# Optimization experiments

Hardware: AMD Instinct MI355X
Metric: run time of the kernel (lower is better)

The kernel has to match this reference:

```python
import jax, jax.numpy as jnp
import numpy as np

B, N, C = 8, 4096, 512
H, DK, DV = 8, 64, 64


def _xnorm(x, gamma):
    # L2 norm over last dim, keepdim; scale by per-head gamma
    nrm = jnp.sqrt(jnp.sum(x * x, axis=-1, keepdims=True))
    return x * gamma / nrm


def setup_inputs() -> dict:
    key = jax.random.key(0)
    ks = jax.random.split(key, 9)
    inp = {
        "queries": jax.random.normal(ks[0], (B, N, C), dtype=jnp.float32),
        "keys": jax.random.normal(ks[1], (B, N, C), dtype=jnp.float32),
        "values": jax.random.normal(ks[2], (B, N, C), dtype=jnp.float32),
        # Linear weights stored torch-style [out, in]; init.normal_(std=0.001), bias=0
        "Wq": jax.random.normal(ks[3], (H * DK, C), dtype=jnp.float32) * 0.001,
        "bq": jnp.zeros((H * DK,), dtype=jnp.float32),
        "Wk": jax.random.normal(ks[4], (H * DK, C), dtype=jnp.float32) * 0.001,
        "bk": jnp.zeros((H * DK,), dtype=jnp.float32),
        "Wv": jax.random.normal(ks[5], (H * DV, C), dtype=jnp.float32) * 0.001,
        "bv": jnp.zeros((H * DV,), dtype=jnp.float32),
        "Wo": jax.random.normal(ks[6], (C, H * DV), dtype=jnp.float32) * 0.001,
        "bo": jnp.zeros((C,), dtype=jnp.float32),
        "gamma": jax.random.normal(ks[7], (1, H, 1, 1), dtype=jnp.float32),
    }
    return inp


def reference(queries, keys, values, Wq, bq, Wk, bk, Wv, bv, Wo, bo, gamma):
    bs, nq, _ = queries.shape
    nk = keys.shape[1]
    # projections -> [b, h, n, d]
    q = (queries @ Wq.T + bq).reshape(bs, nq, H, DK).transpose(0, 2, 1, 3)
    k = (keys @ Wk.T + bk).reshape(bs, nk, H, DK).transpose(0, 2, 1, 3)
    v = (values @ Wv.T + bv).reshape(bs, nk, H, DV).transpose(0, 2, 1, 3)
    # kv: [b, h, dk, dv]  (small intermediate)
    kv = jnp.einsum('bhnk,bhnv->bhkv', k, v)
    kv_n = _xnorm(kv, gamma)     # norm over dv
    q_n = _xnorm(q, gamma)       # norm over dk
    out = jnp.einsum('bhnk,bhkv->bhnv', q_n, kv_n)  # [b,h,nq,dv]
    out = out.transpose(0, 2, 1, 3).reshape(bs, nq, H * DV)
    return out @ Wo.T + bo
```

## Files before the change

### kernel.cpp

```cpp
#include <hip/hip_runtime.h>


typedef __attribute__((ext_vector_type(4))) float f32x4;
typedef __attribute__((ext_vector_type(8))) short s16x8;
typedef __attribute__((ext_vector_type(4))) unsigned short u16x4;
typedef __attribute__((ext_vector_type(2))) unsigned u32x2;

#define DEVFN __device__ __forceinline__

DEVFN unsigned short f2b(float f) {
  union { float f; unsigned u; } un; un.f = f;
  unsigned r = un.u + 0x7fffu + ((un.u >> 16) & 1u);
  return (unsigned short)(r >> 16);
}
DEVFN float b2f(unsigned short us) {
  union { unsigned u; float f; } un; un.u = ((unsigned)us) << 16;
  return un.f;
}
DEVFN unsigned pk2(float x0, float x1) {
  union { float f; unsigned u; } a, b;
  a.f = x0; b.f = x1;
  return __builtin_amdgcn_perm(b.u + 0x8000u, a.u + 0x8000u, 0x07060302u);
}

DEVFN void gl_lds16(const void* g, void* l) {
  __builtin_amdgcn_global_load_lds(
      (const __attribute__((address_space(1))) unsigned*)g,
      (__attribute__((address_space(3))) unsigned*)l, 16, 0, 0);
}

template <bool AF32, typename CT>
DEVFN void gemm_core(const void* Ain, const unsigned short* Bt,
                     const float* bias, CT* C, bool qnorm, const float* gamma,
                     int bx, int by) {
  constexpr int NN = 512;
  __shared__ __align__(16) char AsL[2][8192];
  __shared__ __align__(16) char BsL[2][8192];
  const int tid = threadIdx.x, lane = tid & 63, wid = tid >> 6;
  const int wm = (wid >> 1) * 64, wn = (wid & 1) * 64;
  const int r = lane & 15, g = lane >> 4;

  const char* Bsrc = (const char*)Bt +
      (long)(by * 128 + wid * 32 + (lane >> 2)) * 1024 +
      (((lane & 3) ^ ((lane >> 3) & 3)) * 16);

  const char* AsrcR = nullptr;
  const char* AsrcG = nullptr;
  int awr[4];
  if constexpr (AF32) {
    AsrcR = (const char*)Ain + (long)(bx * 128 + (tid >> 1)) * 2048 +
            (tid & 1) * 64;
    const int row = tid >> 1, rs = (row >> 1) & 3;
#pragma unroll
    for (int j = 0; j < 4; ++j) {
      int p = (tid & 1) * 4 + j;
      awr[j] = row * 64 + ((((p >> 1) ^ rs) << 4) | ((p & 1) * 8));
    }
  } else {
    AsrcG = (const char*)Ain +
        (long)(bx * 128 + wid * 32 + (lane >> 2)) * 1024 +
        (((lane & 3) ^ ((lane >> 3) & 3)) * 16);
  }

  f32x4 PA[4];
  f32x4 acc[4][4] = {};

#define ISSUE_A(KT)                                                            \
  {                                                                            \
    _Pragma("unroll") for (int j = 0; j < 4; ++j)                              \
        PA[j] = *reinterpret_cast<const f32x4*>(AsrcR + (KT)*128 + j * 16);    \
  }

#define PACK_WRITE_A(BUF)                                                      \
  {                                                                            \
    _Pragma("unroll") for (int j = 0; j < 4; ++j) {                            \
      u32x2 w;                                                                 \
      w[0] = pk2(PA[j][0], PA[j][1]);                                          \
      w[1] = pk2(PA[j][2], PA[j][3]);                                          \
      *reinterpret_cast<u32x2*>(AsL[BUF] + awr[j]) = w;                        \
    }                                                                          \
  }

#define STAGE_B(BUF, KT)                                                       \
  {                                                                            \
    _Pragma("unroll") for (int q = 0; q < 2; ++q)                              \
        gl_lds16(Bsrc + q * 16384 + (KT)*64,                                   \
                 BsL[BUF] + (wid * 2 + q) * 1024);                             \
  }

#define STAGE_AG(BUF, KT)                                                      \
  {                                                                            \
    _Pragma("unroll") for (int q = 0; q < 2; ++q)                              \
        gl_lds16(AsrcG + q * 16384 + (KT)*64,                                  \
                 AsL[BUF] + (wid * 2 + q) * 1024);                             \
  }

#define COMPUTE(BUF)                                                           \
  {                                                                            \
    s16x8 a[4], b[4];                                                          \
    _Pragma("unroll") for (int i = 0; i < 4; ++i) {                            \
      int ar = wm + i * 16 + r;                                                \
      a[i] = *reinterpret_cast<const s16x8*>(                                  \
          AsL[BUF] + ar * 64 + ((g ^ ((ar >> 1) & 3)) << 4));                  \
      int br = wn + i * 16 + r;                                                \
      b[i] = *reinterpret_cast<const s16x8*>(                                  \
          BsL[BUF] + br * 64 + ((g ^ ((br >> 1) & 3)) << 4));                  \
    }                                                                          \
    _Pragma("unroll") for (int i = 0; i < 4; ++i)                              \
        _Pragma("unroll") for (int j = 0; j < 4; ++j) acc[i][j] =              \
        __builtin_amdgcn_mfma_f32_16x16x32_bf16(a[i], b[j], acc[i][j], 0, 0,   \
                                                0);                            \
  }

#define STEP(CUR, NXT, KT)                                                     \
  if constexpr (AF32) { ISSUE_A(KT) }                                          \
  STAGE_B(NXT, KT)                                                             \
  if constexpr (!AF32) { STAGE_AG(NXT, KT) }                                   \
  COMPUTE(CUR)                                                                 \
  if constexpr (AF32) { PACK_WRITE_A(NXT) }                                    \
  __syncthreads();

  if constexpr (AF32) { ISSUE_A(0) PACK_WRITE_A(0) } else { STAGE_AG(0, 0) }
  STAGE_B(0, 0)
  __syncthreads();

  STEP(0, 1, 1)
  STEP(1, 0, 2)
  STEP(0, 1, 3)
  STEP(1, 0, 4)
  STEP(0, 1, 5)
  STEP(1, 0, 6)
  STEP(0, 1, 7)
  STEP(1, 0, 8)
  STEP(0, 1, 9)
  STEP(1, 0, 10)
  STEP(0, 1, 11)
  STEP(1, 0, 12)
  STEP(0, 1, 13)
  STEP(1, 0, 14)
  STEP(0, 1, 15)
  COMPUTE(1)

#undef ISSUE_A
#undef PACK_WRITE_A
#undef STAGE_B
#undef STAGE_AG
#undef COMPUTE
#undef STEP

  const int crow0 = bx * 128 + wm + g * 4;
  const int ccol0 = by * 128 + wn + r;
#pragma unroll
  for (int j = 0; j < 4; ++j) {
    float bv = bias[ccol0 + j * 16];
#pragma unroll
    for (int i = 0; i < 4; ++i)
#pragma unroll
      for (int ii = 0; ii < 4; ++ii) acc[i][j][ii] += bv;
  }
  if (qnorm) {
    const int h = (by * 128 + wn) >> 6;
    const float gam = gamma[h];
#pragma unroll
    for (int i = 0; i < 4; ++i)
#pragma unroll
      for (int ii = 0; ii < 4; ++ii) {
        float s = 0.f;
#pragma unroll
        for (int j = 0; j < 4; ++j) s += acc[i][j][ii] * acc[i][j][ii];
        s += __shfl_xor(s, 1);
        s += __shfl_xor(s, 2);
        s += __shfl_xor(s, 4);
        s += __shfl_xor(s, 8);
        float sc = gam / sqrtf(s);
#pragma unroll
        for (int j = 0; j < 4; ++j) acc[i][j][ii] *= sc;
      }
  }
#pragma unroll
  for (int i = 0; i < 4; ++i)
#pragma unroll
    for (int j = 0; j < 4; ++j)
#pragma unroll
      for (int ii = 0; ii < 4; ++ii) {
        long row = crow0 + i * 16 + ii;
        int col = ccol0 + j * 16;
        if constexpr (sizeof(CT) == 2)
          C[row * NN + col] = f2b(acc[i][j][ii]);
        else
          C[row * NN + col] = acc[i][j][ii];
      }
}

DEVFN void swz_xy(int bid, int nwg, int& bx, int& by) {
  int s = (bid & 7) * (nwg >> 3) + (bid >> 3);
  bx = s >> 2;
  by = s & 3;
}

__global__ __launch_bounds__(256, 3)
void proj_qkv(const float* __restrict__ Aq, const float* __restrict__ Ak,
              const float* __restrict__ Av, const unsigned short* __restrict__ Bq,
              const unsigned short* __restrict__ Bk, const unsigned short* __restrict__ Bv,
              const float* __restrict__ bq, const float* __restrict__ bk,
              const float* __restrict__ bv, unsigned short* __restrict__ Cq,
              unsigned short* __restrict__ Ck, unsigned short* __restrict__ Cv,
              const float* __restrict__ gamma) {
  const int z = blockIdx.z;
  const float* A = z == 0 ? Aq : (z == 1 ? Ak : Av);
  const unsigned short* B = z == 0 ? Bq : (z == 1 ? Bk : Bv);
  const float* bias = z == 0 ? bq : (z == 1 ? bk : bv);
  unsigned short* C = z == 0 ? Cq : (z == 1 ? Ck : Cv);
  int bx, by;
  swz_xy(blockIdx.x, 1024, bx, by);
  gemm_core<true, unsigned short>(A, B, bias, C, z == 0, gamma, bx, by);
}

__global__ __launch_bounds__(256, 3)
void gemm_final(const unsigned short* __restrict__ q, const unsigned short* __restrict__ Mt,
                const float* __restrict__ bo, float* __restrict__ out) {
  const int zb = blockIdx.z;
  int bx, by;
  swz_xy(blockIdx.x, 128, bx, by);
  gemm_core<false, float>(q + (long)zb * 2097152, Mt + (long)zb * 262144, bo,
                          out + (long)zb * 2097152, false, nullptr, bx, by);
}

#define NCHUNK 16
__global__ __launch_bounds__(256, 2)
void kv_partial(const unsigned short* __restrict__ kq,
                const unsigned short* __restrict__ vq,
                float* __restrict__ part) {
  const int tid = threadIdx.x;
  const int chunk = blockIdx.x;
  const int bh = blockIdx.y;
  const int b = bh >> 3, h = bh & 7;
  __shared__ float ks[32][64];
  __shared__ float vs[32][64];
  const int dk0 = (tid & 15) * 4;
  const int dv0 = (tid >> 4) * 4;
  float acc[4][4] = {};
  const long nbase = (long)b * 4096 + chunk * 256;

  for (int sub = 0; sub < 8; ++sub) {
    long n0 = nbase + sub * 32;
#pragma unroll
    for (int i = 0; i < 2; ++i) {
      int e = i * 256 + tid;
      int row = e >> 4, c4 = e & 15;
      long gofs = (n0 + row) * 512 + h * 64 + c4 * 4;
      u16x4 kk = *reinterpret_cast<const u16x4*>(kq + gofs);
      u16x4 vv = *reinterpret_cast<const u16x4*>(vq + gofs);
      f32x4 kf = {b2f(kk[0]), b2f(kk[1]), b2f(kk[2]), b2f(kk[3])};
      f32x4 vf = {b2f(vv[0]), b2f(vv[1]), b2f(vv[2]), b2f(vv[3])};
      *reinterpret_cast<f32x4*>(&ks[row][c4 * 4]) = kf;
      *reinterpret_cast<f32x4*>(&vs[row][c4 * 4]) = vf;
    }
    __syncthreads();
#pragma unroll 4
    for (int n = 0; n < 32; ++n) {
      f32x4 kk = *reinterpret_cast<const f32x4*>(&ks[n][dk0]);
      f32x4 vv = *reinterpret_cast<const f32x4*>(&vs[n][dv0]);
#pragma unroll
      for (int a = 0; a < 4; ++a)
#pragma unroll
        for (int c = 0; c < 4; ++c)
          acc[a][c] += kk[a] * vv[c];
    }
    __syncthreads();
  }
  float* pg = part + ((long)chunk * 64 + bh) * 4096;
#pragma unroll
  for (int a = 0; a < 4; ++a) {
    f32x4 o = {acc[a][0], acc[a][1], acc[a][2], acc[a][3]};
    *reinterpret_cast<f32x4*>(pg + (dk0 + a) * 64 + dv0) = o;
  }
}

__global__ __launch_bounds__(256)
void kv_normN(const float* __restrict__ part, const float* __restrict__ gamma,
              unsigned short* __restrict__ kvn) {
  const int bh = blockIdx.x, h = bh & 7;
  const int tid = threadIdx.x;
  __shared__ float kvs[4096];
  __shared__ float scale[64];
#pragma unroll
  for (int i = 0; i < 4; ++i) {
    int e4 = i * 256 + tid;
    const float* p = part + (long)bh * 4096 + e4 * 4;
    f32x4 s = {0.f, 0.f, 0.f, 0.f};
#pragma unroll
    for (int c = 0; c < NCHUNK; ++c) {
      f32x4 v = *reinterpret_cast<const f32x4*>(p + (long)c * 64 * 4096);
      s += v;
    }
    *reinterpret_cast<f32x4*>(kvs + e4 * 4) = s;
  }
  __syncthreads();
  if (tid < 64) {
    float s = 0.f;
    for (int dv = 0; dv < 64; ++dv) { float x = kvs[tid * 64 + dv]; s += x * x; }
    scale[tid] = gamma[h] / sqrtf(s);
  }
  __syncthreads();
#pragma unroll
  for (int i = 0; i < 4; ++i) {
    int e4 = i * 256 + tid;
    float sc = scale[e4 >> 4];
    f32x4 v = *reinterpret_cast<const f32x4*>(kvs + e4 * 4);
    u16x4 o = {f2b(v[0] * sc), f2b(v[1] * sc), f2b(v[2] * sc), f2b(v[3] * sc)};
    *reinterpret_cast<u16x4*>(kvn + (long)bh * 4096 + e4 * 4) = o;
  }
}

__global__ __launch_bounds__(64)
void mt_kernel(const unsigned short* __restrict__ Wo_b,
               const unsigned short* __restrict__ kvn,
               unsigned short* __restrict__ Mt) {
  const int bid = blockIdx.x;
  const int bh = bid >> 2, seg = bid & 3;
  const int b = bh >> 3, h = bh & 7;
  const int lane = threadIdx.x;
  const int r = lane & 15, g = lane >> 4;
  f32x4 acc[8][4] = {};
  s16x8 bf[2][4];
#pragma unroll
  for (int ks = 0; ks < 2; ++ks)
#pragma unroll
    for (int j = 0; j < 4; ++j)
      bf[ks][j] = *reinterpret_cast<const s16x8*>(
          kvn + (long)bh * 4096 + (j * 16 + r) * 64 + ks * 32 + g * 8);
#pragma unroll
  for (int ks = 0; ks < 2; ++ks)
#pragma unroll
    for (int i = 0; i < 8; ++i) {
      s16x8 af = *reinterpret_cast<const s16x8*>(
          Wo_b + (long)(seg * 128 + i * 16 + r) * 512 + h * 64 + ks * 32 + g * 8);
#pragma unroll
      for (int j = 0; j < 4; ++j)
        acc[i][j] = __builtin_amdgcn_mfma_f32_16x16x32_bf16(af, bf[ks][j], acc[i][j], 0, 0, 0);
    }
#pragma unroll
  for (int i = 0; i < 8; ++i)
#pragma unroll
    for (int j = 0; j < 4; ++j)
#pragma unroll
      for (int ii = 0; ii < 4; ++ii) {
        int c = seg * 128 + i * 16 + g * 4 + ii;
        int dk = j * 16 + r;
        Mt[(long)b * 262144 + (long)c * 512 + h * 64 + dk] = f2b(acc[i][j][ii]);
      }
}

__global__ void cast4(const float* __restrict__ a0, const float* __restrict__ a1,
                      const float* __restrict__ a2, const float* __restrict__ a3,
                      unsigned short* __restrict__ o0, unsigned short* __restrict__ o1,
                      unsigned short* __restrict__ o2, unsigned short* __restrict__ o3) {
  const int y = blockIdx.y;
  const float* in = y == 0 ? a0 : (y == 1 ? a1 : (y == 2 ? a2 : a3));
  unsigned short* out = y == 0 ? o0 : (y == 1 ? o1 : (y == 2 ? o2 : o3));
  int i = blockIdx.x * 256 + threadIdx.x;
  f32x4 v = reinterpret_cast<const f32x4*>(in)[i];
  reinterpret_cast<u16x4*>(out)[i] = u16x4{f2b(v[0]), f2b(v[1]), f2b(v[2]), f2b(v[3])};
}

extern "C" void kernel_launch(void* const* d_in, const int* in_sizes, int n_in,
                              void* d_out, int out_size, void* d_ws, size_t ws_size,
                              hipStream_t stream) {
  const float* queries = (const float*)d_in[0];
  const float* keys    = (const float*)d_in[1];
  const float* values  = (const float*)d_in[2];
  const float* Wq = (const float*)d_in[3];
  const float* bq = (const float*)d_in[4];
  const float* Wk = (const float*)d_in[5];
  const float* bk = (const float*)d_in[6];
  const float* Wv = (const float*)d_in[7];
  const float* bv = (const float*)d_in[8];
  const float* Wo = (const float*)d_in[9];
  const float* bo = (const float*)d_in[10];
  const float* gamma = (const float*)d_in[11];

  unsigned short* Wq_b = (unsigned short*)d_ws;
  unsigned short* Wk_b = Wq_b + 262144;
  unsigned short* Wv_b = Wk_b + 262144;
  unsigned short* Wo_b = Wv_b + 262144;
  unsigned short* q_b  = Wo_b + 262144;
  unsigned short* kvn  = q_b + 16777216;
  float* part = (float*)(kvn + 262144);
  unsigned short* Mt = (unsigned short*)part;
  unsigned short* k_b = (unsigned short*)d_out;
  unsigned short* v_b = k_b + 16777216;
  float* out = (float*)d_out;

  cast4<<<dim3(256, 4), 256, 0, stream>>>(Wq, Wk, Wv, Wo, Wq_b, Wk_b, Wv_b, Wo_b);

  proj_qkv<<<dim3(1024, 1, 3), 256, 0, stream>>>(
      queries, keys, values, Wq_b, Wk_b, Wv_b, bq, bk, bv, q_b, k_b, v_b, gamma);

  kv_partial<<<dim3(NCHUNK, 64), 256, 0, stream>>>(k_b, v_b, part);
  kv_normN<<<64, 256, 0, stream>>>(part, gamma, kvn);
  mt_kernel<<<256, 64, 0, stream>>>(Wo_b, kvn, Mt);

  gemm_final<<<dim3(128, 1, 8), 256, 0, stream>>>(q_b, Mt, bo, out);
}
```

Before: 204.2 us.

## Use full-N 128x512 GEMM tiles with 1024-thread blocks for projections and output

Replaces the 128x128 GEMM tile with a 128x512 tile that covers all output columns, run by 16 waves per block. Each row block of the fp32 activations is now loaded and converted to bf16 once, instead of once per 128-column tile, which removes redundant global reads and packing work. The k-loop becomes a rolled loop, and the block swizzle is dropped. In exchange, LDS per block is much larger (80 KB), only one block fits per CU, and the 1024-thread launch bound caps registers, which risks spills and leaves fewer blocks to hide latency.

```diff
diff --git a/kernel.cpp b/kernel.cpp
--- a/kernel.cpp
+++ b/kernel.cpp
@@ -22,7 +22,6 @@
   a.f = x0; b.f = x1;
   return __builtin_amdgcn_perm(b.u + 0x8000u, a.u + 0x8000u, 0x07060302u);
 }
-
 DEVFN void gl_lds16(const void* g, void* l) {
   __builtin_amdgcn_global_load_lds(
       (const __attribute__((address_space(1))) unsigned*)g,
@@ -30,81 +29,60 @@
 }
 
 template <bool AF32, typename CT>
-DEVFN void gemm_core(const void* Ain, const unsigned short* Bt,
-                     const float* bias, CT* C, bool qnorm, const float* gamma,
-                     int bx, int by) {
-  constexpr int NN = 512;
-  __shared__ __align__(16) char AsL[2][8192];
-  __shared__ __align__(16) char BsL[2][8192];
+DEVFN void gemmN512(const void* Ain, const unsigned short* Bt,
+                    const float* bias, CT* C, bool qnorm,
+                    const float* gamma, int bx) {
+  __shared__ __align__(16) char LA[2][8192];
+  __shared__ __align__(16) char LB[2][32768];
   const int tid = threadIdx.x, lane = tid & 63, wid = tid >> 6;
-  const int wm = (wid >> 1) * 64, wn = (wid & 1) * 64;
   const int r = lane & 15, g = lane >> 4;
-
-  const char* Bsrc = (const char*)Bt +
-      (long)(by * 128 + wid * 32 + (lane >> 2)) * 1024 +
-      (((lane & 3) ^ ((lane >> 3) & 3)) * 16);
-
-  const char* AsrcR = nullptr;
-  const char* AsrcG = nullptr;
-  int awr[4];
+  const int mw = wid >> 3;
+  const int nw = wid & 7;
+
+  const char* BsS = (const char*)Bt + (long)(wid * 32 + (lane >> 2)) * 1024 +
+                    (((lane & 3) ^ ((lane >> 3) & 3)) * 16);
+
+  const char* AfS = nullptr;
+  const char* AsS = nullptr;
+  int awr = 0;
   if constexpr (AF32) {
-    AsrcR = (const char*)Ain + (long)(bx * 128 + (tid >> 1)) * 2048 +
-            (tid & 1) * 64;
-    const int row = tid >> 1, rs = (row >> 1) & 3;
-#pragma unroll
-    for (int j = 0; j < 4; ++j) {
-      int p = (tid & 1) * 4 + j;
-      awr[j] = row * 64 + ((((p >> 1) ^ rs) << 4) | ((p & 1) * 8));
-    }
+    AfS = (const char*)Ain + (long)(bx * 128 + (tid >> 3)) * 2048 +
+          (tid & 7) * 16;
+    const int row = tid >> 3, p = tid & 7;
+    awr = row * 64 + (((p >> 1) ^ ((row >> 1) & 3)) << 4) + (p & 1) * 8;
   } else {
-    AsrcG = (const char*)Ain +
-        (long)(bx * 128 + wid * 32 + (lane >> 2)) * 1024 +
-        (((lane & 3) ^ ((lane >> 3) & 3)) * 16);
-  }
-
-  f32x4 PA[4];
+    AsS = (const char*)Ain + (long)(bx * 128 + wid * 16 + (lane >> 2)) * 1024 +
+          (((lane & 3) ^ ((lane >> 3) & 3)) * 16);
+  }
+
   f32x4 acc[4][4] = {};
-
-#define ISSUE_A(KT)                                                            \
+  f32x4 pa;
+
+#define SGB(BUF, KT)                                                           \
+  gl_lds16(BsS + (KT)*64, LB[BUF] + wid * 2048);                               \
+  gl_lds16(BsS + 16384 + (KT)*64, LB[BUF] + wid * 2048 + 1024);
+#define SGA(BUF, KT)                                                           \
+  if (wid < 8) { gl_lds16(AsS + (KT)*64, LA[BUF] + wid * 1024); }
+#define LDA(KT) pa = *reinterpret_cast<const f32x4*>(AfS + (KT)*128);
+#define WRA(BUF)                                                               \
   {                                                                            \
-    _Pragma("unroll") for (int j = 0; j < 4; ++j)                              \
-        PA[j] = *reinterpret_cast<const f32x4*>(AsrcR + (KT)*128 + j * 16);    \
-  }
-
-#define PACK_WRITE_A(BUF)                                                      \
-  {                                                                            \
-    _Pragma("unroll") for (int j = 0; j < 4; ++j) {                            \
-      u32x2 w;                                                                 \
-      w[0] = pk2(PA[j][0], PA[j][1]);                                          \
-      w[1] = pk2(PA[j][2], PA[j][3]);                                          \
-      *reinterpret_cast<u32x2*>(AsL[BUF] + awr[j]) = w;                        \
-    }                                                                          \
-  }
-
-#define STAGE_B(BUF, KT)                                                       \
-  {                                                                            \
-    _Pragma("unroll") for (int q = 0; q < 2; ++q)                              \
-        gl_lds16(Bsrc + q * 16384 + (KT)*64,                                   \
-                 BsL[BUF] + (wid * 2 + q) * 1024);                             \
-  }
-
-#define STAGE_AG(BUF, KT)                                                      \
-  {                                                                            \
-    _Pragma("unroll") for (int q = 0; q < 2; ++q)                              \
-        gl_lds16(AsrcG + q * 16384 + (KT)*64,                                  \
-                 AsL[BUF] + (wid * 2 + q) * 1024);                             \
-  }
-
+    u32x2 w;                                                                   \
+    w[0] = pk2(pa[0], pa[1]);                                                  \
+    w[1] = pk2(pa[2], pa[3]);                                                  \
+    *reinterpret_cast<u32x2*>(LA[BUF] + awr) = w;                              \
+  }
 #define COMPUTE(BUF)                                                           \
   {                                                                            \
     s16x8 a[4], b[4];                                                          \
     _Pragma("unroll") for (int i = 0; i < 4; ++i) {                            \
-      int ar = wm + i * 16 + r;                                                \
+      int ar = mw * 64 + i * 16 + r;                                           \
       a[i] = *reinterpret_cast<const s16x8*>(                                  \
-          AsL[BUF] + ar * 64 + ((g ^ ((ar >> 1) & 3)) << 4));                  \
-      int br = wn + i * 16 + r;                                                \
-      b[i] = *reinterpret_cast<const s16x8*>(                                  \
-          BsL[BUF] + br * 64 + ((g ^ ((br >> 1) & 3)) << 4));                  \
+          LA[BUF] + ar * 64 + ((g ^ ((ar >> 1) & 3)) << 4));                   \
+    }                                                                          \
+    _Pragma("unroll") for (int j = 0; j < 4; ++j) {                            \
+      int br = nw * 64 + j * 16 + r;                                           \
+      b[j] = *reinterpret_cast<const s16x8*>(                                  \
+          LB[BUF] + br * 64 + ((g ^ ((br >> 1) & 3)) << 4));                   \
     }                                                                          \
     _Pragma("unroll") for (int i = 0; i < 4; ++i)                              \
         _Pragma("unroll") for (int j = 0; j < 4; ++j) acc[i][j] =              \
@@ -112,44 +90,34 @@
                                                 0);                            \
   }
 
-#define STEP(CUR, NXT, KT)                                                     \
-  if constexpr (AF32) { ISSUE_A(KT) }                                          \
-  STAGE_B(NXT, KT)                                                             \
-  if constexpr (!AF32) { STAGE_AG(NXT, KT) }                                   \
-  COMPUTE(CUR)                                                                 \
-  if constexpr (AF32) { PACK_WRITE_A(NXT) }                                    \
+  if constexpr (AF32) {
+    LDA(0) WRA(0)
+  } else {
+    SGA(0, 0)
+  }
+  SGB(0, 0)
   __syncthreads();
 
-  if constexpr (AF32) { ISSUE_A(0) PACK_WRITE_A(0) } else { STAGE_AG(0, 0) }
-  STAGE_B(0, 0)
-  __syncthreads();
-
-  STEP(0, 1, 1)
-  STEP(1, 0, 2)
-  STEP(0, 1, 3)
-  STEP(1, 0, 4)
-  STEP(0, 1, 5)
-  STEP(1, 0, 6)
-  STEP(0, 1, 7)
-  STEP(1, 0, 8)
-  STEP(0, 1, 9)
-  STEP(1, 0, 10)
-  STEP(0, 1, 11)
-  STEP(1, 0, 12)
-  STEP(0, 1, 13)
-  STEP(1, 0, 14)
-  STEP(0, 1, 15)
+#pragma unroll 1
+  for (int t = 0; t < 15; ++t) {
+    const int cur = t & 1, nxt = cur ^ 1;
+    if constexpr (AF32) { LDA(t + 1) }
+    SGB(nxt, t + 1)
+    if constexpr (!AF32) { SGA(nxt, t + 1) }
+    COMPUTE(cur)
+    if constexpr (AF32) { WRA(nxt) }
+    __syncthreads();
+  }
   COMPUTE(1)
 
-#undef ISSUE_A
-#undef PACK_WRITE_A
-#undef STAGE_B
-#undef STAGE_AG
+#undef SGB
+#undef SGA
+#undef LDA
+#undef WRA
 #undef COMPUTE
-#undef STEP
-
-  const int crow0 = bx * 128 + wm + g * 4;
-  const int ccol0 = by * 128 + wn + r;
+
+  const int crow0 = bx * 128 + mw * 64 + g * 4;
+  const int ccol0 = nw * 64 + r;
 #pragma unroll
   for (int j = 0; j < 4; ++j) {
     float bv = bias[ccol0 + j * 16];
@@ -159,8 +127,7 @@
       for (int ii = 0; ii < 4; ++ii) acc[i][j][ii] += bv;
   }
   if (qnorm) {
-    const int h = (by * 128 + wn) >> 6;
-    const float gam = gamma[h];
+    const float gam = gamma[nw];
 #pragma unroll
     for (int i = 0; i < 4; ++i)
 #pragma unroll
@@ -186,19 +153,13 @@
         long row = crow0 + i * 16 + ii;
         int col = ccol0 + j * 16;
         if constexpr (sizeof(CT) == 2)
-          C[row * NN + col] = f2b(acc[i][j][ii]);
+          C[row * 512 + col] = f2b(acc[i][j][ii]);
         else
-          C[row * NN + col] = acc[i][j][ii];
+          C[row * 512 + col] = acc[i][j][ii];
       }
 }
 
-DEVFN void swz_xy(int bid, int nwg, int& bx, int& by) {
-  int s = (bid & 7) * (nwg >> 3) + (bid >> 3);
-  bx = s >> 2;
-  by = s & 3;
-}
-
-__global__ __launch_bounds__(256, 3)
+__global__ __launch_bounds__(1024)
 void proj_qkv(const float* __restrict__ Aq, const float* __restrict__ Ak,
               const float* __restrict__ Av, const unsigned short* __restrict__ Bq,
               const unsigned short* __restrict__ Bk, const unsigned short* __restrict__ Bv,
@@ -206,24 +167,20 @@
               const float* __restrict__ bv, unsigned short* __restrict__ Cq,
               unsigned short* __restrict__ Ck, unsigned short* __restrict__ Cv,
               const float* __restrict__ gamma) {
-  const int z = blockIdx.z;
+  const int z = blockIdx.y;
   const float* A = z == 0 ? Aq : (z == 1 ? Ak : Av);
   const unsigned short* B = z == 0 ? Bq : (z == 1 ? Bk : Bv);
   const float* bias = z == 0 ? bq : (z == 1 ? bk : bv);
   unsigned short* C = z == 0 ? Cq : (z == 1 ? Ck : Cv);
-  int bx, by;
-  swz_xy(blockIdx.x, 1024, bx, by);
-  gemm_core<true, unsigned short>(A, B, bias, C, z == 0, gamma, bx, by);
-}
-
-__global__ __launch_bounds__(256, 3)
+  gemmN512<true, unsigned short>(A, B, bias, C, z == 0, gamma, blockIdx.x);
+}
+
+__global__ __launch_bounds__(1024)
 void gemm_final(const unsigned short* __restrict__ q, const unsigned short* __restrict__ Mt,
                 const float* __restrict__ bo, float* __restrict__ out) {
-  const int zb = blockIdx.z;
-  int bx, by;
-  swz_xy(blockIdx.x, 128, bx, by);
-  gemm_core<false, float>(q + (long)zb * 2097152, Mt + (long)zb * 262144, bo,
-                          out + (long)zb * 2097152, false, nullptr, bx, by);
+  const int zb = blockIdx.y;
+  gemmN512<false, float>(q + (long)zb * 2097152, Mt + (long)zb * 262144, bo,
+                         out + (long)zb * 2097152, false, nullptr, blockIdx.x);
 }
 
 #define NCHUNK 16
@@ -394,12 +351,12 @@
 
   cast4<<<dim3(256, 4), 256, 0, stream>>>(Wq, Wk, Wv, Wo, Wq_b, Wk_b, Wv_b, Wo_b);
 
-  proj_qkv<<<dim3(1024, 1, 3), 256, 0, stream>>>(
+  proj_qkv<<<dim3(256, 3), 1024, 0, stream>>>(
       queries, keys, values, Wq_b, Wk_b, Wv_b, bq, bk, bv, q_b, k_b, v_b, gamma);
 
   kv_partial<<<dim3(NCHUNK, 64), 256, 0, stream>>>(k_b, v_b, part);
   kv_normN<<<64, 256, 0, stream>>>(part, gamma, kvn);
   mt_kernel<<<256, 64, 0, stream>>>(Wo_b, kvn, Mt);
 
-  gemm_final<<<dim3(128, 1, 8), 256, 0, stream>>>(q_b, Mt, bo, out);
-}
+  gemm_final<<<dim3(32, 8), 1024, 0, stream>>>(q_b, Mt, bo, out);
+}
```

After: 174.6 us. 1.17x faster.
